# Performance work log

Measured on AMD Instinct MI355X. Metric: run time of the kernel, lower is better.

Reference implementation:

```python
import jax, jax.numpy as jnp
import numpy as np
import math

EPS = 1e-8
MIN_RADIUS = 0.1
SINH_MAX = math.asinh(2.0 ** 15)
CURV = 1.0                     # exp(clamp(log(1.0), log(0.1), log(10)))
IMAGE_ALPHA = 0.25             # exp(clamp(log(1/4), max=0))
TEXT_ALPHA = 1.0 / 0.6         # exp(log(1/0.6)), frozen
LOGIT_SCALE = 1.0 / 0.07       # exp(clamp(log(1/0.07), max=4.6052))
ENTAIL_WEIGHT = 0.2


def exp_map0(x, curv):
    # MERU exponential map at the Lorentz-model origin (space components only).
    rc = jnp.sqrt(curv) * jnp.linalg.norm(x, axis=-1, keepdims=True)
    sinh_in = jnp.clip(rc, EPS, SINH_MAX)
    return jnp.sinh(sinh_in) * x / jnp.maximum(rc, EPS)


def pairwise_dist(x, y, curv):
    # x: (B,H,W,D) image feats on hyperboloid; y: (C,D) text protos. -> (B,H,W,C)
    x_time = jnp.sqrt(1.0 / curv + jnp.sum(x * x, axis=-1))   # (B,H,W)
    y_time = jnp.sqrt(1.0 / curv + jnp.sum(y * y, axis=-1))   # (C,)
    inner = jnp.einsum('bhwd,cd->bhwc', x, y) - x_time[..., None] * y_time
    c_xyl = -curv * inner
    return jnp.arccosh(jnp.maximum(c_xyl, 1.0 + EPS)) / jnp.sqrt(curv)


def oxy_angle(x, y, curv):
    # Exterior angle at x between origin->x and x->y geodesics. x,y: (...,D) -> (...,)
    x_time = jnp.sqrt(1.0 / curv + jnp.sum(x * x, axis=-1))
    y_time = jnp.sqrt(1.0 / curv + jnp.sum(y * y, axis=-1))
    c_xyl = curv * (jnp.sum(x * y, axis=-1) - x_time * y_time)
    acos_num = y_time + c_xyl * x_time
    acos_den = jnp.linalg.norm(x, axis=-1) * jnp.sqrt(jnp.maximum(c_xyl * c_xyl - 1.0, 0.0))
    acos_in = acos_num / (acos_den + EPS)
    return jnp.arccos(jnp.clip(acos_in, -1.0 + EPS, 1.0 - EPS))


def half_aperture(x, curv):
    asin_in = 2.0 * MIN_RADIUS / (jnp.linalg.norm(x, axis=-1) * jnp.sqrt(curv) + EPS)
    return jnp.arcsin(jnp.clip(asin_in, -1.0 + EPS, 1.0 - EPS))


def _forward(feats, text_protos, labels, mask):
    curv = jnp.float32(CURV)
    img = exp_map0(feats * IMAGE_ALPHA, curv)          # (B,H,W,D)
    txt = exp_map0(text_protos * TEXT_ALPHA, curv)     # (C,D)

    dist = pairwise_dist(img, txt, curv)               # (B,H,W,C)
    proto = txt[labels]                                # (B,H,W,D) gather by GT class
    angle = oxy_angle(proto, img, curv)                # (B,H,W)
    aperture = half_aperture(proto, curv)              # (B,H,W)

    logits = LOGIT_SCALE * (-dist)                     # scale * image_logits
    logp = jax.nn.log_softmax(logits, axis=-1)
    nll = -jnp.take_along_axis(logp, labels[..., None], axis=-1)[..., 0]

    valid = (~mask).astype(jnp.float32)                # mask==1 means ignore
    n_valid = jnp.maximum(jnp.sum(valid), 1.0)
    sup_loss = jnp.sum(nll * valid) / n_valid

    ent = jnp.maximum(angle - aperture, 0.0)
    entail_loss = jnp.sum(ent * valid) / n_valid

    return sup_loss + ENTAIL_WEIGHT * entail_loss


def setup_inputs() -> dict:
    key = jax.random.key(0)
    k1, k2, k3, k4 = jax.random.split(key, 4)
    B, H, W, D, C = 2, 512, 512, 64, 151
    feats = jax.random.normal(k1, (B, H, W, D), dtype=jnp.float32)
    text_protos = jax.random.normal(k2, (C, D), dtype=jnp.float32)
    labels = jax.random.randint(k3, (B, H, W), 0, C, dtype=jnp.int32)
    mask = jax.random.randint(k4, (B, H, W), 0, 2, dtype=jnp.int32).astype(bool)
    return {"feats": feats, "text_protos": text_protos, "labels": labels, "mask": mask}


def reference(feats, text_protos, labels, mask):
    return _forward(feats, text_protos, labels, mask)
```

## Files before the change

### kernel.cpp

```cpp
#include <hip/hip_runtime.h>
#include <math.h>

#define EPSF 1e-8f
#define SINH_MAXF 11.090354888959125f
#define IMAGE_ALPHA 0.25f
#define TEXT_ALPHA (1.0f/0.6f)
#define LOGIT_SCALE (1.0f/0.07f)
#define LN2F 0.6931471805599453f
#define SLN (LOGIT_SCALE*LN2F)
#define ENTAIL_WEIGHT 0.2f
#define NCLS 151
#define NPAD 160
#define DIM 64
#define NBLK 4096

#define LMIN_OFF 8
#define YT_OFF 16
#define XN_OFF (YT_OFF + NPAD)
#define AP_OFF (XN_OFF + NPAD)
#define BT_OFF 512
#define BLK_OFF (BT_OFF + NPAD*DIM/2)

typedef __attribute__((ext_vector_type(8))) short bf16x8;
typedef __attribute__((ext_vector_type(4))) float f32x4;

__device__ inline unsigned short f2bf(float f) {
    unsigned int u = __float_as_uint(f);
    return (unsigned short)((u + 0x7FFFu + ((u >> 16) & 1u)) >> 16);
}
__device__ inline unsigned int pack_bf_trunc(float hi, float lo) {
    return __builtin_amdgcn_perm(__float_as_uint(hi), __float_as_uint(lo), 0x07060302u);
}
__device__ inline float sel4(const float* a, int i) {
    return i == 0 ? a[0] : i == 1 ? a[1] : i == 2 ? a[2] : a[3];
}
__device__ inline int isel4(const int* a, int i) {
    return i == 0 ? a[0] : i == 1 ? a[1] : i == 2 ? a[2] : a[3];
}

__global__ __launch_bounds__(256) void proto_kernel(const float* __restrict__ protos,
                                                    float* __restrict__ ws) {
    int tid = threadIdx.x, w = tid >> 6, l = tid & 63;
    unsigned short* bt = (unsigned short*)(ws + BT_OFF);
    __shared__ float sYT[NPAD];
    for (int c = w; c < NPAD; c += 4) {
        int t = c >> 4, cn = c & 15;
        int half = l >> 5, g = (l >> 3) & 3, j = l & 7;
        int sidx = (t * 128 + half * 64 + g * 16 + cn) * 8 + j;
        float yt_c;
        if (c < NCLS) {
            float v = protos[c * DIM + l] * TEXT_ALPHA;
            float n2 = v * v;
            #pragma unroll
            for (int m = 32; m >= 1; m >>= 1) n2 += __shfl_xor(n2, m, 64);
            float rc = __builtin_amdgcn_sqrtf(n2);
            float rr = fminf(fmaxf(rc, EPSF), SINH_MAXF);
            float e = __expf(rr);
            float sh = 0.5f * (e - __builtin_amdgcn_rcpf(e));
            float sc = sh * __builtin_amdgcn_rcpf(fmaxf(rc, EPSF));
            bt[sidx] = f2bf(sc * v);
            float xn = sc * rc;
            yt_c = __builtin_amdgcn_sqrtf(fmaf(xn, xn, 1.f));
            if (l == 0) {
                ws[YT_OFF + c] = yt_c;
                ws[XN_OFF + c] = xn;
                float ai = fminf(fmaxf(0.2f / (xn + EPSF), -1.f + EPSF), 1.f - EPSF);
                ws[AP_OFF + c] = asinf(ai);
            }
        } else {
            bt[sidx] = 0;
            yt_c = 2e18f;
            if (l == 0) { ws[YT_OFF + c] = 2e18f; ws[XN_OFF + c] = 1.f; ws[AP_OFF + c] = 0.f; }
        }
        if (l == 0) sYT[c] = yt_c;
    }
    __syncthreads();
    if (tid < 64) {
        float m = 1e30f;
        for (int c = tid; c < NCLS; c += 64) m = fminf(m, sYT[c]);
        #pragma unroll
        for (int k = 32; k >= 1; k >>= 1) m = fminf(m, __shfl_xor(m, k, 64));
        if (tid == 0) ws[LMIN_OFF] = __log2f(2.f * m);
    }
}

struct PixA { bf16x8 q0, q1; float xt, Q; };

__device__ inline PixA stage_pixel(const float4* fp, float lmin2) {
    float4 f0 = fp[0], f1 = fp[1], f2 = fp[8], f3 = fp[9];
    float n2r = f0.x*f0.x + f0.y*f0.y + f0.z*f0.z + f0.w*f0.w
              + f1.x*f1.x + f1.y*f1.y + f1.z*f1.z + f1.w*f1.w
              + f2.x*f2.x + f2.y*f2.y + f2.z*f2.z + f2.w*f2.w
              + f3.x*f3.x + f3.y*f3.y + f3.z*f3.z + f3.w*f3.w;
    n2r += __shfl_xor(n2r, 16, 64);
    n2r += __shfl_xor(n2r, 32, 64);
    float rc = IMAGE_ALPHA * __builtin_amdgcn_sqrtf(n2r);
    float rr = fminf(fmaxf(rc, EPSF), SINH_MAXF);
    float e = __expf(rr);
    float sh = 0.5f * (e - __builtin_amdgcn_rcpf(e));
    float sc = sh * __builtin_amdgcn_rcpf(fmaxf(rc, EPSF));
    float xn = sc * rc;
    float k = sc * IMAGE_ALPHA;
    PixA r;
    r.xt = __builtin_amdgcn_sqrtf(fmaf(xn, xn, 1.f));
    r.Q = SLN * (lmin2 - __log2f(r.xt + xn)) - SLN;
    unsigned int* q0u = (unsigned int*)&r.q0;
    unsigned int* q1u = (unsigned int*)&r.q1;
    q0u[0] = pack_bf_trunc(k*f0.y, k*f0.x);
    q0u[1] = pack_bf_trunc(k*f0.w, k*f0.z);
    q0u[2] = pack_bf_trunc(k*f1.y, k*f1.x);
    q0u[3] = pack_bf_trunc(k*f1.w, k*f1.z);
    q1u[0] = pack_bf_trunc(k*f2.y, k*f2.x);
    q1u[1] = pack_bf_trunc(k*f2.w, k*f2.z);
    q1u[2] = pack_bf_trunc(k*f3.y, k*f3.x);
    q1u[3] = pack_bf_trunc(k*f3.w, k*f3.z);
    return r;
}

__global__ __launch_bounds__(256) void main_kernel(
    const float* __restrict__ feats, const int* __restrict__ labels,
    const unsigned char* __restrict__ mask, const float* __restrict__ wsro,
    float4* __restrict__ blkout)
{
    __shared__ uint4 sBT[1280];
    __shared__ float sYT[NPAD];
    int tid = threadIdx.x;
    const uint4* btg = (const uint4*)(wsro + BT_OFF);
    #pragma unroll
    for (int k = 0; k < 5; k++) sBT[tid + k * 256] = btg[tid + k * 256];
    if (tid < NPAD) sYT[tid] = wsro[YT_OFF + tid];
    __syncthreads();

    int wid = tid >> 6, lane = tid & 63;
    int cn = lane & 15, g = lane >> 4;
    int wavebase = (blockIdx.x * 4 + wid) * 32;
    int pix0 = wavebase + cn, pix1 = pix0 + 16;
    float lmin2 = wsro[LMIN_OFF];

    PixA A0 = stage_pixel((const float4*)(feats + (size_t)pix0 * DIM + g * 8), lmin2);
    PixA A1 = stage_pixel((const float4*)(feats + (size_t)pix1 * DIM + g * 8), lmin2);
    int lab0 = labels[pix0], lab1 = labels[pix1];

    float xtr0[4], Q0[4], xtr1[4], Q1[4];
    int lr0[4], lr1[4];
    #pragma unroll
    for (int r = 0; r < 4; r++) {
        int src = g * 4 + r;
        xtr0[r] = __shfl(A0.xt, src, 64); Q0[r] = __shfl(A0.Q, src, 64);
        lr0[r]  = __shfl(lab0, src, 64);
        xtr1[r] = __shfl(A1.xt, src, 64); Q1[r] = __shfl(A1.Q, src, 64);
        lr1[r]  = __shfl(lab1, src, 64);
    }

    float ss0[4] = {0,0,0,0}, ss1[4] = {0,0,0,0};
    float sv0[4] = {0,0,0,0}, sv1[4] = {0,0,0,0};

    #pragma unroll 2
    for (int t = 0; t < 10; t++) {
        uint4 u0 = sBT[t * 128 + lane];
        uint4 u1 = sBT[t * 128 + 64 + lane];
        bf16x8 bq0 = __builtin_bit_cast(bf16x8, u0);
        bf16x8 bq1 = __builtin_bit_cast(bf16x8, u1);
        float yt = sYT[t * 16 + cn];
        int cls = t * 16 + cn;
        f32x4 d0 = {0,0,0,0}, d1 = {0,0,0,0};
        d0 = __builtin_amdgcn_mfma_f32_16x16x32_bf16(A0.q0, bq0, d0, 0, 0, 0);
        d0 = __builtin_amdgcn_mfma_f32_16x16x32_bf16(A0.q1, bq1, d0, 0, 0, 0);
        d1 = __builtin_amdgcn_mfma_f32_16x16x32_bf16(A1.q0, bq0, d1, 0, 0, 0);
        d1 = __builtin_amdgcn_mfma_f32_16x16x32_bf16(A1.q1, bq1, d1, 0, 0, 0);
        #pragma unroll
        for (int r = 0; r < 4; r++) {
            float c0 = fmaf(xtr0[r], yt, -d0[r]);
            if (lr0[r] == cls) sv0[r] = c0;
            ss0[r] += __expf(fmaf(-SLN, __log2f(c0), Q0[r]));
            float c1 = fmaf(xtr1[r], yt, -d1[r]);
            if (lr1[r] == cls) sv1[r] = c1;
            ss1[r] += __expf(fmaf(-SLN, __log2f(c1), Q1[r]));
        }
    }

    int gbase = lane & 48;
    float cx0[4], cx1[4];
    #pragma unroll
    for (int r = 0; r < 4; r++) {
        cx0[r] = __shfl(sv0[r], gbase + (lr0[r] & 15), 64);
        cx1[r] = __shfl(sv1[r], gbase + (lr1[r] & 15), 64);
    }
    #pragma unroll
    for (int k = 1; k < 16; k <<= 1) {
        #pragma unroll
        for (int r = 0; r < 4; r++) {
            ss0[r] += __shfl_xor(ss0[r], k, 64);
            ss1[r] += __shfl_xor(ss1[r], k, 64);
        }
    }

    float v_nll = 0.f, v_ent = 0.f, valid = 0.f;
    if (cn < 4) {
        #pragma unroll
        for (int tile = 0; tile < 2; tile++) {
            float T   = tile ? sel4(ss1, cn) : sel4(ss0, cn);
            float cxl = tile ? sel4(cx1, cn) : sel4(cx0, cn);
            float xts = tile ? sel4(xtr1, cn) : sel4(xtr0, cn);
            float Q   = tile ? sel4(Q1, cn) : sel4(Q0, cn);
            int lb    = tile ? isel4(lr1, cn) : isel4(lr0, cn);
            int pr = wavebase + g * 4 + cn + tile * 16;
            float nll = __logf(T) - Q + SLN * __log2f(cxl);
            float pt = wsro[YT_OFF + lb], pn = wsro[XN_OFF + lb], ap = wsro[AP_OFF + lb];
            float num = fmaf(-cxl, pt, xts);
            float den = pn * __builtin_amdgcn_sqrtf(fmaxf(fmaf(cxl, cxl, -1.f), 0.f));
            float ain = num * __builtin_amdgcn_rcpf(den + EPSF);
            ain = fminf(fmaxf(ain, -1.f + EPSF), 1.f - EPSF);
            float ax = fabsf(ain);
            float p = fmaf(fmaf(fmaf(-0.0187293f, ax, 0.0742610f), ax, -0.2121144f),
                           ax, 1.5707288f);
            float rr = __builtin_amdgcn_sqrtf(1.f - ax) * p;
            float ac = ain < 0.f ? 3.14159265358979f - rr : rr;
            float ent = fmaxf(ac - ap, 0.f);
            float vl = mask[pr] ? 0.f : 1.f;
            v_nll += nll * vl; v_ent += ent * vl; valid += vl;
        }
    }

    #pragma unroll
    for (int o = 32; o >= 1; o >>= 1) {
        v_nll += __shfl_down(v_nll, o, 64);
        v_ent += __shfl_down(v_ent, o, 64);
        valid += __shfl_down(valid, o, 64);
    }
    __shared__ float red[3][4];
    if (lane == 0) { red[0][wid] = v_nll; red[1][wid] = v_ent; red[2][wid] = valid; }
    __syncthreads();
    if (tid == 0) {
        float a = 0.f, b = 0.f, c = 0.f;
        #pragma unroll
        for (int w = 0; w < 4; w++) { a += red[0][w]; b += red[1][w]; c += red[2][w]; }
        blkout[blockIdx.x] = make_float4(a, b, c, 0.f);
    }
}

__global__ __launch_bounds__(1024) void reduce_kernel(const float4* __restrict__ blk,
                                                      float* __restrict__ out) {
    float a = 0.f, b = 0.f, c = 0.f;
    for (int i = threadIdx.x; i < NBLK; i += 1024) {
        float4 v = blk[i];
        a += v.x; b += v.y; c += v.z;
    }
    #pragma unroll
    for (int o = 32; o >= 1; o >>= 1) {
        a += __shfl_down(a, o, 64);
        b += __shfl_down(b, o, 64);
        c += __shfl_down(c, o, 64);
    }
    __shared__ float red[3][16];
    int wid = threadIdx.x >> 6, lane = threadIdx.x & 63;
    if (lane == 0) { red[0][wid] = a; red[1][wid] = b; red[2][wid] = c; }
    __syncthreads();
    if (threadIdx.x == 0) {
        float A = 0.f, B = 0.f, C = 0.f;
        #pragma unroll
        for (int w = 0; w < 16; w++) { A += red[0][w]; B += red[1][w]; C += red[2][w]; }
        float n = fmaxf(C, 1.f);
        out[0] = A / n + ENTAIL_WEIGHT * (B / n);
    }
}

extern "C" void kernel_launch(void* const* d_in, const int* in_sizes, int n_in,
                              void* d_out, int out_size, void* d_ws, size_t ws_size,
                              hipStream_t stream) {
    const float* feats  = (const float*)d_in[0];
    const float* protos = (const float*)d_in[1];
    const int* labels   = (const int*)d_in[2];
    const unsigned char* mask = (const unsigned char*)d_in[3];
    float* ws = (float*)d_ws;

    proto_kernel<<<1, 256, 0, stream>>>(protos, ws);

    int npix = in_sizes[2];
    int nblk = npix / 128;
    main_kernel<<<nblk, 256, 0, stream>>>(feats, labels, mask, ws,
                                          (float4*)(ws + BLK_OFF));
    reduce_kernel<<<1, 1024, 0, stream>>>((const float4*)(ws + BLK_OFF), (float*)d_out);
}
```

Measured before the change: 236.9 us.

## Fuse final reduction into main kernel via last-block atomic, use exp2 in softmax

Removes the separate reduce kernel launch by having each block atomically increment a counter and the last block perform the final sum. The proto kernel is restructured so 16-lane groups load float4 prototypes and write packed bf16 pairs, and it resets the counter. The inner loop switches from expf with a pre-multiplied ln2 to a native exp2, which saves a multiply per class per pixel. The atomic adds a serialization point at the end of the grid and relies on the counter being reset every call.

```diff
diff --git a/kernel.cpp b/kernel.cpp
--- a/kernel.cpp
+++ b/kernel.cpp
@@ -14,6 +14,7 @@
 #define DIM 64
 #define NBLK 4096
 
+#define CNT_OFF 4
 #define LMIN_OFF 8
 #define YT_OFF 16
 #define XN_OFF (YT_OFF + NPAD)
@@ -21,6 +22,12 @@
 #define BT_OFF 512
 #define BLK_OFF (BT_OFF + NPAD*DIM/2)
 
+#if __has_builtin(__builtin_amdgcn_exp2f)
+#define EXP2F(x) __builtin_amdgcn_exp2f(x)
+#else
+#define EXP2F(x) __expf((x) * LN2F)
+#endif
+
 typedef __attribute__((ext_vector_type(8))) short bf16x8;
 typedef __attribute__((ext_vector_type(4))) float f32x4;
 
@@ -40,40 +47,46 @@
 
 __global__ __launch_bounds__(256) void proto_kernel(const float* __restrict__ protos,
                                                     float* __restrict__ ws) {
-    int tid = threadIdx.x, w = tid >> 6, l = tid & 63;
-    unsigned short* bt = (unsigned short*)(ws + BT_OFF);
+    int tid = threadIdx.x;
+    int grp = tid >> 4, li = tid & 15;
+    unsigned int* btu = (unsigned int*)(ws + BT_OFF);
     __shared__ float sYT[NPAD];
-    for (int c = w; c < NPAD; c += 4) {
-        int t = c >> 4, cn = c & 15;
-        int half = l >> 5, g = (l >> 3) & 3, j = l & 7;
-        int sidx = (t * 128 + half * 64 + g * 16 + cn) * 8 + j;
-        float yt_c;
+    #pragma unroll 2
+    for (int t = 0; t < 10; t++) {
+        int c = t * 16 + grp;
+        float4 p4 = make_float4(0.f, 0.f, 0.f, 0.f);
+        if (c < NCLS) p4 = ((const float4*)protos)[c * 16 + li];
+        float vx = p4.x * TEXT_ALPHA, vy = p4.y * TEXT_ALPHA,
+              vz = p4.z * TEXT_ALPHA, vw = p4.w * TEXT_ALPHA;
+        float n2 = vx*vx + vy*vy + vz*vz + vw*vw;
+        #pragma unroll
+        for (int m = 8; m >= 1; m >>= 1) n2 += __shfl_xor(n2, m, 64);
+        float rc = __builtin_amdgcn_sqrtf(n2);
+        float rr = fminf(fmaxf(rc, EPSF), SINH_MAXF);
+        float e = __expf(rr);
+        float sh = 0.5f * (e - __builtin_amdgcn_rcpf(e));
+        float sc = sh * __builtin_amdgcn_rcpf(fmaxf(rc, EPSF));
+        unsigned int u0, u1;
+        float yt, xn, ap;
         if (c < NCLS) {
-            float v = protos[c * DIM + l] * TEXT_ALPHA;
-            float n2 = v * v;
-            #pragma unroll
-            for (int m = 32; m >= 1; m >>= 1) n2 += __shfl_xor(n2, m, 64);
-            float rc = __builtin_amdgcn_sqrtf(n2);
-            float rr = fminf(fmaxf(rc, EPSF), SINH_MAXF);
-            float e = __expf(rr);
-            float sh = 0.5f * (e - __builtin_amdgcn_rcpf(e));
-            float sc = sh * __builtin_amdgcn_rcpf(fmaxf(rc, EPSF));
-            bt[sidx] = f2bf(sc * v);
-            float xn = sc * rc;
-            yt_c = __builtin_amdgcn_sqrtf(fmaf(xn, xn, 1.f));
-            if (l == 0) {
-                ws[YT_OFF + c] = yt_c;
-                ws[XN_OFF + c] = xn;
-                float ai = fminf(fmaxf(0.2f / (xn + EPSF), -1.f + EPSF), 1.f - EPSF);
-                ws[AP_OFF + c] = asinf(ai);
-            }
+            u0 = (unsigned int)f2bf(sc * vx) | ((unsigned int)f2bf(sc * vy) << 16);
+            u1 = (unsigned int)f2bf(sc * vz) | ((unsigned int)f2bf(sc * vw) << 16);
+            xn = sc * rc;
+            yt = __builtin_amdgcn_sqrtf(fmaf(xn, xn, 1.f));
+            float ai = fminf(fmaxf(0.2f / (xn + EPSF), -1.f + EPSF), 1.f - EPSF);
+            ap = asinf(ai);
         } else {
-            bt[sidx] = 0;
-            yt_c = 2e18f;
-            if (l == 0) { ws[YT_OFF + c] = 2e18f; ws[XN_OFF + c] = 1.f; ws[AP_OFF + c] = 0.f; }
-        }
-        if (l == 0) sYT[c] = yt_c;
-    }
+            u0 = 0u; u1 = 0u; yt = 2e18f; xn = 1.f; ap = 0.f;
+        }
+        int unit = t * 128 + (li >> 3) * 64 + ((li >> 1) & 3) * 16 + grp;
+        btu[unit * 4 + (li & 1) * 2]     = u0;
+        btu[unit * 4 + (li & 1) * 2 + 1] = u1;
+        if (li == 0) {
+            ws[YT_OFF + c] = yt; ws[XN_OFF + c] = xn; ws[AP_OFF + c] = ap;
+            sYT[c] = yt;
+        }
+    }
+    if (tid == 0) ((unsigned int*)ws)[CNT_OFF] = 0u;
     __syncthreads();
     if (tid < 64) {
         float m = 1e30f;
@@ -103,7 +116,7 @@
     float k = sc * IMAGE_ALPHA;
     PixA r;
     r.xt = __builtin_amdgcn_sqrtf(fmaf(xn, xn, 1.f));
-    r.Q = SLN * (lmin2 - __log2f(r.xt + xn)) - SLN;
+    r.Q = LOGIT_SCALE * (lmin2 - __log2f(r.xt + xn) - 1.0f);
     unsigned int* q0u = (unsigned int*)&r.q0;
     unsigned int* q1u = (unsigned int*)&r.q1;
     q0u[0] = pack_bf_trunc(k*f0.y, k*f0.x);
@@ -120,7 +133,8 @@
 __global__ __launch_bounds__(256) void main_kernel(
     const float* __restrict__ feats, const int* __restrict__ labels,
     const unsigned char* __restrict__ mask, const float* __restrict__ wsro,
-    float4* __restrict__ blkout)
+    float4* __restrict__ blkout, unsigned int* __restrict__ cnt,
+    float* __restrict__ out)
 {
     __shared__ uint4 sBT[1280];
     __shared__ float sYT[NPAD];
@@ -172,10 +186,10 @@
         for (int r = 0; r < 4; r++) {
             float c0 = fmaf(xtr0[r], yt, -d0[r]);
             if (lr0[r] == cls) sv0[r] = c0;
-            ss0[r] += __expf(fmaf(-SLN, __log2f(c0), Q0[r]));
+            ss0[r] += EXP2F(fmaf(-LOGIT_SCALE, __log2f(c0), Q0[r]));
             float c1 = fmaf(xtr1[r], yt, -d1[r]);
             if (lr1[r] == cls) sv1[r] = c1;
-            ss1[r] += __expf(fmaf(-SLN, __log2f(c1), Q1[r]));
+            ss1[r] += EXP2F(fmaf(-LOGIT_SCALE, __log2f(c1), Q1[r]));
         }
     }
 
@@ -205,7 +219,7 @@
             float Q   = tile ? sel4(Q1, cn) : sel4(Q0, cn);
             int lb    = tile ? isel4(lr1, cn) : isel4(lr0, cn);
             int pr = wavebase + g * 4 + cn + tile * 16;
-            float nll = __logf(T) - Q + SLN * __log2f(cxl);
+            float nll = LN2F * (__log2f(T) - Q + LOGIT_SCALE * __log2f(cxl));
             float pt = wsro[YT_OFF + lb], pn = wsro[XN_OFF + lb], ap = wsro[AP_OFF + lb];
             float num = fmaf(-cxl, pt, xts);
             float den = pn * __builtin_amdgcn_sqrtf(fmaxf(fmaf(cxl, cxl, -1.f), 0.f));
@@ -229,6 +243,7 @@
         valid += __shfl_down(valid, o, 64);
     }
     __shared__ float red[3][4];
+    __shared__ bool amLast;
     if (lane == 0) { red[0][wid] = v_nll; red[1][wid] = v_ent; red[2][wid] = valid; }
     __syncthreads();
     if (tid == 0) {
@@ -236,32 +251,35 @@
         #pragma unroll
         for (int w = 0; w < 4; w++) { a += red[0][w]; b += red[1][w]; c += red[2][w]; }
         blkout[blockIdx.x] = make_float4(a, b, c, 0.f);
-    }
-}
-
-__global__ __launch_bounds__(1024) void reduce_kernel(const float4* __restrict__ blk,
-                                                      float* __restrict__ out) {
-    float a = 0.f, b = 0.f, c = 0.f;
-    for (int i = threadIdx.x; i < NBLK; i += 1024) {
-        float4 v = blk[i];
-        a += v.x; b += v.y; c += v.z;
-    }
-    #pragma unroll
-    for (int o = 32; o >= 1; o >>= 1) {
-        a += __shfl_down(a, o, 64);
-        b += __shfl_down(b, o, 64);
-        c += __shfl_down(c, o, 64);
-    }
-    __shared__ float red[3][16];
-    int wid = threadIdx.x >> 6, lane = threadIdx.x & 63;
-    if (lane == 0) { red[0][wid] = a; red[1][wid] = b; red[2][wid] = c; }
+        __threadfence();
+        unsigned int old = atomicAdd(cnt, 1u);
+        amLast = (old == gridDim.x - 1);
+    }
     __syncthreads();
-    if (threadIdx.x == 0) {
-        float A = 0.f, B = 0.f, C = 0.f;
-        #pragma unroll
-        for (int w = 0; w < 16; w++) { A += red[0][w]; B += red[1][w]; C += red[2][w]; }
-        float n = fmaxf(C, 1.f);
-        out[0] = A / n + ENTAIL_WEIGHT * (B / n);
+    if (amLast) {
+        __threadfence();
+        float a = 0.f, b = 0.f, c = 0.f;
+        int nb = gridDim.x;
+        for (int i = tid; i < nb; i += 256) {
+            float4 v = blkout[i];
+            a += v.x; b += v.y; c += v.z;
+        }
+        #pragma unroll
+        for (int o = 32; o >= 1; o >>= 1) {
+            a += __shfl_down(a, o, 64);
+            b += __shfl_down(b, o, 64);
+            c += __shfl_down(c, o, 64);
+        }
+        __shared__ float fr[3][4];
+        if (lane == 0) { fr[0][wid] = a; fr[1][wid] = b; fr[2][wid] = c; }
+        __syncthreads();
+        if (tid == 0) {
+            float A = fr[0][0] + fr[0][1] + fr[0][2] + fr[0][3];
+            float B = fr[1][0] + fr[1][1] + fr[1][2] + fr[1][3];
+            float C = fr[2][0] + fr[2][1] + fr[2][2] + fr[2][3];
+            float n = fmaxf(C, 1.f);
+            out[0] = A / n + ENTAIL_WEIGHT * (B / n);
+        }
     }
 }
 
@@ -279,6 +297,7 @@
     int npix = in_sizes[2];
     int nblk = npix / 128;
     main_kernel<<<nblk, 256, 0, stream>>>(feats, labels, mask, ws,
-                                          (float4*)(ws + BLK_OFF));
-    reduce_kernel<<<1, 1024, 0, stream>>>((const float4*)(ws + BLK_OFF), (float*)d_out);
-}
+                                          (float4*)(ws + BLK_OFF),
+                                          (unsigned int*)(ws + CNT_OFF),
+                                          (float*)d_out);
+}
```

New measurement: 478.8 us. 2.02x slower.
